# Performance work log

Hardware: AMD Instinct MI355X
Metric: run time of the kernel (lower is better)

Reference implementation:

```python
import jax, jax.numpy as jnp
import numpy as np

BS = 1024        # BATCH_SIZE
IA = 3           # INPUT_AXIS
A = BS * IA      # 3072
D = BS * (IA - 1)  # 2048


def _linear(x, w, b):
    # torch Linear: y = x @ W^T + b, W is [out, in]
    return x @ w.T + b


def _pdist_flat(a):
    # a: [BS, d] -> flat [BS*BS] pairwise Euclidean distances.
    # The original adds min(a) to both coords; it cancels in the difference.
    d2 = jnp.sum((a[:, None, :] - a[None, :, :]) ** 2, axis=-1)  # [BS, BS]
    return jnp.sqrt(d2).reshape(-1)


def setup_inputs() -> dict:
    key = jax.random.key(0)
    ks = jax.random.split(key, 17)
    s = 0.02
    inp = {"x": jax.random.normal(ks[0], (A,), dtype=jnp.float32)}
    # encoder: Linear(A,A), Linear(A,A), Linear(A,A), Linear(A,D)
    enc_shapes = [(A, A), (A, A), (A, A), (D, A)]
    # decoder: Linear(D,A), Linear(A,A), Linear(A,A), Linear(A,A)
    dec_shapes = [(A, D), (A, A), (A, A), (A, A)]
    i = 1
    for j, (o, n) in enumerate(enc_shapes, 1):
        inp[f"ew{j}"] = jax.random.normal(ks[i], (o, n), dtype=jnp.float32) * s; i += 1
        inp[f"eb{j}"] = jnp.zeros((o,), dtype=jnp.float32)
    for j, (o, n) in enumerate(dec_shapes, 1):
        inp[f"dw{j}"] = jax.random.normal(ks[i], (o, n), dtype=jnp.float32) * s; i += 1
        inp[f"db{j}"] = jnp.zeros((o,), dtype=jnp.float32)
    return inp


def reference(x, ew1, eb1, ew2, eb2, ew3, eb3, ew4, eb4,
              dw1, db1, dw2, db2, dw3, db3, dw4, db4):
    # encoder: Lin+Tanh, Lin+Tanh, Lin, Lin, Tanhshrink
    h = jnp.tanh(_linear(x, ew1, eb1))
    h = jnp.tanh(_linear(h, ew2, eb2))
    h = _linear(h, ew3, eb3)
    h = _linear(h, ew4, eb4)
    y = h - jnp.tanh(h)  # Tanhshrink, shape [D]

    in_data = x.reshape(BS, IA)
    lat_repr = y.reshape(BS, IA - 1)

    in_diff_sum = jax.lax.stop_gradient(_pdist_flat(in_data))    # [BS*BS]
    lat_diff_sum = jax.lax.stop_gradient(_pdist_flat(lat_repr))  # [BS*BS]

    # decoder: Lin+Tanh, Lin+Tanh, Lin, Lin, Tanh
    g = jnp.tanh(_linear(y, dw1, db1))
    g = jnp.tanh(_linear(g, dw2, db2))
    g = _linear(g, dw3, db3)
    g = _linear(g, dw4, db4)
    output = jnp.tanh(g)  # [A]

    return (output, in_diff_sum, lat_diff_sum, lat_repr)
```

## Files before the change

### kernel.cpp

```cpp
#include <hip/hip_runtime.h>
#include <math.h>

#define BS 1024
#define AA 3072
#define DD 2048

template<int IN_DIM, int ACT>
__global__ __launch_bounds__(256) void matvec_act(
    const float* __restrict__ W, const float* __restrict__ b,
    const float* __restrict__ x, float* __restrict__ y,
    float* __restrict__ y2, int out_dim)
{
    int row  = (int)((blockIdx.x * blockDim.x + threadIdx.x) >> 6);
    int lane = (int)(threadIdx.x & 63);
    if (row >= out_dim) return;

    const float4* __restrict__ Wr = (const float4*)(W + (size_t)row * IN_DIM);
    const float4* __restrict__ xv = (const float4*)x;

    constexpr int N4 = IN_DIM / 4;
    float sum = 0.f;
#pragma unroll
    for (int it = 0; it < N4 / 64; ++it) {
        int i = lane + it * 64;
        float4 w4 = Wr[i];
        float4 x4 = xv[i];
        sum += w4.x * x4.x + w4.y * x4.y + w4.z * x4.z + w4.w * x4.w;
    }

#pragma unroll
    for (int off = 32; off; off >>= 1) sum += __shfl_down(sum, off);

    if (lane == 0) {
        float v = sum + b[row];
        if (ACT == 1)      v = tanhf(v);
        else if (ACT == 2) v = v - tanhf(v);
        y[row] = v;
        if (y2) y2[row] = v;
    }
}

__global__ __launch_bounds__(256) void pdist3_kernel(
    const float* __restrict__ a, float* __restrict__ out)
{
    int idx = (int)(blockIdx.x * blockDim.x + threadIdx.x);
    int i = idx >> 10, j = idx & 1023;
    float d0 = a[3 * i + 0] - a[3 * j + 0];
    float d1 = a[3 * i + 1] - a[3 * j + 1];
    float d2 = a[3 * i + 2] - a[3 * j + 2];
    out[idx] = sqrtf(d0 * d0 + d1 * d1 + d2 * d2);
}

__global__ __launch_bounds__(256) void pdist2_kernel(
    const float* __restrict__ a, float* __restrict__ out)
{
    int idx = (int)(blockIdx.x * blockDim.x + threadIdx.x);
    int i = idx >> 10, j = idx & 1023;
    float d0 = a[2 * i + 0] - a[2 * j + 0];
    float d1 = a[2 * i + 1] - a[2 * j + 1];
    out[idx] = sqrtf(d0 * d0 + d1 * d1);
}

extern "C" void kernel_launch(void* const* d_in, const int* in_sizes, int n_in,
                              void* d_out, int out_size, void* d_ws, size_t ws_size,
                              hipStream_t stream)
{
    const float* x   = (const float*)d_in[0];
    const float* ew1 = (const float*)d_in[1];  const float* eb1 = (const float*)d_in[2];
    const float* ew2 = (const float*)d_in[3];  const float* eb2 = (const float*)d_in[4];
    const float* ew3 = (const float*)d_in[5];  const float* eb3 = (const float*)d_in[6];
    const float* ew4 = (const float*)d_in[7];  const float* eb4 = (const float*)d_in[8];
    const float* dw1 = (const float*)d_in[9];  const float* db1 = (const float*)d_in[10];
    const float* dw2 = (const float*)d_in[11]; const float* db2 = (const float*)d_in[12];
    const float* dw3 = (const float*)d_in[13]; const float* db3 = (const float*)d_in[14];
    const float* dw4 = (const float*)d_in[15]; const float* db4 = (const float*)d_in[16];

    float* out      = (float*)d_out;
    float* out_y    = out;
    float* out_ind  = out + AA;
    float* out_lat  = out_ind + BS * BS;
    float* out_rep  = out_lat + BS * BS;

    float* ws = (float*)d_ws;
    float* h1 = ws;
    float* h2 = h1 + AA;
    float* h3 = h2 + AA;
    float* yy = h3 + AA;
    float* g1 = yy + DD;
    float* g2 = g1 + AA;
    float* g3 = g2 + AA;

    dim3 blk(256);

    pdist3_kernel<<<BS * BS / 256, blk, 0, stream>>>(x, out_ind);

    matvec_act<AA, 1><<<AA / 4, blk, 0, stream>>>(ew1, eb1, x,  h1, nullptr, AA);
    matvec_act<AA, 1><<<AA / 4, blk, 0, stream>>>(ew2, eb2, h1, h2, nullptr, AA);
    matvec_act<AA, 0><<<AA / 4, blk, 0, stream>>>(ew3, eb3, h2, h3, nullptr, AA);
    matvec_act<AA, 2><<<DD / 4, blk, 0, stream>>>(ew4, eb4, h3, yy, out_rep, DD);

    pdist2_kernel<<<BS * BS / 256, blk, 0, stream>>>(yy, out_lat);

    matvec_act<DD, 1><<<AA / 4, blk, 0, stream>>>(dw1, db1, yy, g1, nullptr, AA);
    matvec_act<AA, 1><<<AA / 4, blk, 0, stream>>>(dw2, db2, g1, g2, nullptr, AA);
    matvec_act<AA, 0><<<AA / 4, blk, 0, stream>>>(dw3, db3, g2, g3, nullptr, AA);
    matvec_act<AA, 1><<<AA / 4, blk, 0, stream>>>(dw4, db4, g3, out_y, nullptr, AA);
}
```

Baseline: 293.3 us.

## Fuse all layers into persistent kernel with grid barriers and weight prefetch

Replaces the ten separate kernel launches with one persistent kernel of 768 blocks, one wave per output row, synchronised by an atomic grid barrier between layers. Each wave prefetches the next layer's weight row into registers while computing the current dot product, so weight streaming overlaps the barrier waits. The pairwise-distance outputs are spread across idle waves and co-scheduled with the matvec stages. This removes launch gaps and exposed memory latency, but relies on all 768 blocks being co-resident (3 blocks per CU). It also adds heavy register pressure and a barrier with a timeout guard that could silently break synchronisation.

Result: slower. 1.008 ms (+243.5%).

```diff
diff --git a/kernel.cpp b/kernel.cpp
--- a/kernel.cpp
+++ b/kernel.cpp
@@ -4,61 +4,178 @@
 #define BS 1024
 #define AA 3072
 #define DD 2048
-
-template<int IN_DIM, int ACT>
-__global__ __launch_bounds__(256) void matvec_act(
-    const float* __restrict__ W, const float* __restrict__ b,
-    const float* __restrict__ x, float* __restrict__ y,
-    float* __restrict__ y2, int out_dim)
+#define NBLK 768
+#define NTHR 256
+#define NWAVES (NBLK * (NTHR / 64))
+
+__device__ __forceinline__ float wave_reduce(float s) {
+#pragma unroll
+    for (int off = 32; off; off >>= 1) s += __shfl_down(s, off);
+    return s;
+}
+
+template<int N4>
+__device__ __forceinline__ void load_row(float4* f, const float* __restrict__ W,
+                                         int row, int in_dim, int lane) {
+    const float4* p = (const float4*)(W + (size_t)row * in_dim);
+#pragma unroll
+    for (int i = 0; i < N4; ++i) f[i] = p[lane + i * 64];
+}
+
+template<int N4>
+__device__ __forceinline__ float dot_row(const float4* f, const float* __restrict__ xp, int lane) {
+    const float4* xv = (const float4*)xp;
+    float s = 0.f;
+#pragma unroll
+    for (int i = 0; i < N4; ++i) {
+        float4 x4 = xv[lane + i * 64];
+        s += f[i].x * x4.x + f[i].y * x4.y + f[i].z * x4.z + f[i].w * x4.w;
+    }
+    return s;
+}
+
+__device__ __forceinline__ void grid_bar(unsigned* cnt, unsigned target) {
+    __syncthreads();
+    if (threadIdx.x == 0) {
+        __threadfence();
+        __hip_atomic_fetch_add(cnt, 1u, __ATOMIC_RELEASE, __HIP_MEMORY_SCOPE_AGENT);
+        int guard = 0;
+        while (__hip_atomic_load(cnt, __ATOMIC_ACQUIRE, __HIP_MEMORY_SCOPE_AGENT) < target) {
+            __builtin_amdgcn_s_sleep(8);
+            if (++guard > 4000000) break;
+        }
+    }
+    __syncthreads();
+}
+
+__global__ __launch_bounds__(NTHR, 3) void fused_ae(
+    const float* __restrict__ x,
+    const float* __restrict__ ew1, const float* __restrict__ eb1,
+    const float* __restrict__ ew2, const float* __restrict__ eb2,
+    const float* __restrict__ ew3, const float* __restrict__ eb3,
+    const float* __restrict__ ew4, const float* __restrict__ eb4,
+    const float* __restrict__ dw1, const float* __restrict__ db1,
+    const float* __restrict__ dw2, const float* __restrict__ db2,
+    const float* __restrict__ dw3, const float* __restrict__ db3,
+    const float* __restrict__ dw4, const float* __restrict__ db4,
+    float* __restrict__ out_y, float* __restrict__ out_ind,
+    float* __restrict__ out_lat, float* __restrict__ out_rep,
+    float* __restrict__ h1, float* __restrict__ h2, float* __restrict__ h3,
+    float* __restrict__ yy, float* __restrict__ g1, float* __restrict__ g2,
+    float* __restrict__ g3, unsigned* __restrict__ bar)
 {
-    int row  = (int)((blockIdx.x * blockDim.x + threadIdx.x) >> 6);
-    int lane = (int)(threadIdx.x & 63);
-    if (row >= out_dim) return;
-
-    const float4* __restrict__ Wr = (const float4*)(W + (size_t)row * IN_DIM);
-    const float4* __restrict__ xv = (const float4*)x;
-
-    constexpr int N4 = IN_DIM / 4;
-    float sum = 0.f;
-#pragma unroll
-    for (int it = 0; it < N4 / 64; ++it) {
-        int i = lane + it * 64;
-        float4 w4 = Wr[i];
-        float4 x4 = xv[i];
-        sum += w4.x * x4.x + w4.y * x4.y + w4.z * x4.z + w4.w * x4.w;
-    }
-
-#pragma unroll
-    for (int off = 32; off; off >>= 1) sum += __shfl_down(sum, off);
-
-    if (lane == 0) {
-        float v = sum + b[row];
-        if (ACT == 1)      v = tanhf(v);
-        else if (ACT == 2) v = v - tanhf(v);
-        y[row] = v;
-        if (y2) y2[row] = v;
-    }
-}
-
-__global__ __launch_bounds__(256) void pdist3_kernel(
-    const float* __restrict__ a, float* __restrict__ out)
-{
-    int idx = (int)(blockIdx.x * blockDim.x + threadIdx.x);
-    int i = idx >> 10, j = idx & 1023;
-    float d0 = a[3 * i + 0] - a[3 * j + 0];
-    float d1 = a[3 * i + 1] - a[3 * j + 1];
-    float d2 = a[3 * i + 2] - a[3 * j + 2];
-    out[idx] = sqrtf(d0 * d0 + d1 * d1 + d2 * d2);
-}
-
-__global__ __launch_bounds__(256) void pdist2_kernel(
-    const float* __restrict__ a, float* __restrict__ out)
-{
-    int idx = (int)(blockIdx.x * blockDim.x + threadIdx.x);
-    int i = idx >> 10, j = idx & 1023;
-    float d0 = a[2 * i + 0] - a[2 * j + 0];
-    float d1 = a[2 * i + 1] - a[2 * j + 1];
-    out[idx] = sqrtf(d0 * d0 + d1 * d1);
+    const int wave = blockIdx.x * (NTHR / 64) + (int)(threadIdx.x >> 6);
+    const int lane = (int)(threadIdx.x & 63);
+
+    float4 A[12], B[12];
+
+    load_row<12>(A, ew1, wave, AA, lane);
+
+    {
+        float s = dot_row<12>(A, x, lane);
+        __builtin_amdgcn_sched_barrier(0);
+        load_row<12>(B, ew2, wave, AA, lane);
+        __builtin_amdgcn_sched_barrier(0);
+        s = wave_reduce(s);
+        if (lane == 0) h1[wave] = tanhf(s + eb1[wave]);
+    }
+    grid_bar(bar, 1 * NBLK);
+
+    {
+        float s = dot_row<12>(B, h1, lane);
+        __builtin_amdgcn_sched_barrier(0);
+        load_row<12>(A, ew3, wave, AA, lane);
+        __builtin_amdgcn_sched_barrier(0);
+        s = wave_reduce(s);
+        if (lane == 0) h2[wave] = tanhf(s + eb2[wave]);
+    }
+    grid_bar(bar, 2 * NBLK);
+
+    {
+        float s = dot_row<12>(A, h2, lane);
+        __builtin_amdgcn_sched_barrier(0);
+        if (wave < DD) load_row<12>(B, ew4, wave, AA, lane);
+        __builtin_amdgcn_sched_barrier(0);
+        s = wave_reduce(s);
+        if (lane == 0) h3[wave] = s + eb3[wave];
+    }
+    grid_bar(bar, 3 * NBLK);
+
+    {
+        float s = 0.f;
+        if (wave < DD) s = dot_row<12>(B, h3, lane);
+        __builtin_amdgcn_sched_barrier(0);
+        load_row<8>(A, dw1, wave, DD, lane);
+        __builtin_amdgcn_sched_barrier(0);
+        if (wave < DD) {
+            s = wave_reduce(s);
+            if (lane == 0) {
+                float v = s + eb4[wave];
+                v = v - tanhf(v);
+                yy[wave] = v;
+                out_rep[wave] = v;
+            }
+        } else {
+            int t = (wave - DD) * 64 + lane;
+#pragma unroll
+            for (int k = 0; k < 16; ++k) {
+                int idx = t + k * 65536;
+                int i = idx >> 10, j = idx & 1023;
+                float d0 = x[3 * i + 0] - x[3 * j + 0];
+                float d1 = x[3 * i + 1] - x[3 * j + 1];
+                float d2 = x[3 * i + 2] - x[3 * j + 2];
+                out_ind[idx] = sqrtf(d0 * d0 + d1 * d1 + d2 * d2);
+            }
+        }
+    }
+    grid_bar(bar, 4 * NBLK);
+
+    {
+        float s = dot_row<8>(A, yy, lane);
+        __builtin_amdgcn_sched_barrier(0);
+        load_row<12>(B, dw2, wave, AA, lane);
+        __builtin_amdgcn_sched_barrier(0);
+        s = wave_reduce(s);
+        if (lane == 0) g1[wave] = tanhf(s + db1[wave]);
+        int t = wave * 64 + lane;
+#pragma unroll
+        for (int k = 0; k < 6; ++k) {
+            int idx = t + k * (NWAVES * 64);
+            if (idx < BS * BS) {
+                int i = idx >> 10, j = idx & 1023;
+                float d0 = yy[2 * i + 0] - yy[2 * j + 0];
+                float d1 = yy[2 * i + 1] - yy[2 * j + 1];
+                out_lat[idx] = sqrtf(d0 * d0 + d1 * d1);
+            }
+        }
+    }
+    grid_bar(bar, 5 * NBLK);
+
+    {
+        float s = dot_row<12>(B, g1, lane);
+        __builtin_amdgcn_sched_barrier(0);
+        load_row<12>(A, dw3, wave, AA, lane);
+        __builtin_amdgcn_sched_barrier(0);
+        s = wave_reduce(s);
+        if (lane == 0) g2[wave] = tanhf(s + db2[wave]);
+    }
+    grid_bar(bar, 6 * NBLK);
+
+    {
+        float s = dot_row<12>(A, g2, lane);
+        __builtin_amdgcn_sched_barrier(0);
+        load_row<12>(B, dw4, wave, AA, lane);
+        __builtin_amdgcn_sched_barrier(0);
+        s = wave_reduce(s);
+        if (lane == 0) g3[wave] = s + db3[wave];
+    }
+    grid_bar(bar, 7 * NBLK);
+
+    {
+        float s = dot_row<12>(B, g3, lane);
+        s = wave_reduce(s);
+        if (lane == 0) out_y[wave] = tanhf(s + db4[wave]);
+    }
 }
 
 extern "C" void kernel_launch(void* const* d_in, const int* in_sizes, int n_in,
@@ -75,14 +192,15 @@
     const float* dw3 = (const float*)d_in[13]; const float* db3 = (const float*)d_in[14];
     const float* dw4 = (const float*)d_in[15]; const float* db4 = (const float*)d_in[16];
 
-    float* out      = (float*)d_out;
-    float* out_y    = out;
-    float* out_ind  = out + AA;
-    float* out_lat  = out_ind + BS * BS;
-    float* out_rep  = out_lat + BS * BS;
-
-    float* ws = (float*)d_ws;
-    float* h1 = ws;
+    float* out     = (float*)d_out;
+    float* out_y   = out;
+    float* out_ind = out + AA;
+    float* out_lat = out_ind + BS * BS;
+    float* out_rep = out_lat + BS * BS;
+
+    unsigned* bar = (unsigned*)d_ws;
+    float* act = (float*)((char*)d_ws + 256);
+    float* h1 = act;
     float* h2 = h1 + AA;
     float* h3 = h2 + AA;
     float* yy = h3 + AA;
@@ -90,19 +208,11 @@
     float* g2 = g1 + AA;
     float* g3 = g2 + AA;
 
-    dim3 blk(256);
-
-    pdist3_kernel<<<BS * BS / 256, blk, 0, stream>>>(x, out_ind);
-
-    matvec_act<AA, 1><<<AA / 4, blk, 0, stream>>>(ew1, eb1, x,  h1, nullptr, AA);
-    matvec_act<AA, 1><<<AA / 4, blk, 0, stream>>>(ew2, eb2, h1, h2, nullptr, AA);
-    matvec_act<AA, 0><<<AA / 4, blk, 0, stream>>>(ew3, eb3, h2, h3, nullptr, AA);
-    matvec_act<AA, 2><<<DD / 4, blk, 0, stream>>>(ew4, eb4, h3, yy, out_rep, DD);
-
-    pdist2_kernel<<<BS * BS / 256, blk, 0, stream>>>(yy, out_lat);
-
-    matvec_act<DD, 1><<<AA / 4, blk, 0, stream>>>(dw1, db1, yy, g1, nullptr, AA);
-    matvec_act<AA, 1><<<AA / 4, blk, 0, stream>>>(dw2, db2, g1, g2, nullptr, AA);
-    matvec_act<AA, 0><<<AA / 4, blk, 0, stream>>>(dw3, db3, g2, g3, nullptr, AA);
-    matvec_act<AA, 1><<<AA / 4, blk, 0, stream>>>(dw4, db4, g3, out_y, nullptr, AA);
-}
+    hipMemsetAsync(d_ws, 0, 256, stream);
+
+    fused_ae<<<NBLK, NTHR, 0, stream>>>(
+        x, ew1, eb1, ew2, eb2, ew3, eb3, ew4, eb4,
+        dw1, db1, dw2, db2, dw3, db3, dw4, db4,
+        out_y, out_ind, out_lat, out_rep,
+        h1, h2, h3, yy, g1, g2, g3, bar);
+}
```
